# Performance work log

Measured on AMD Instinct MI355X. Metric: run time of the kernel, lower is better.

The kernel has to match this reference:

```python
import jax, jax.numpy as jnp
import numpy as np

B, D_IN, D_H = 4096, 1024, 1024


def setup_inputs() -> dict:
    key = jax.random.key(0)
    ks = jax.random.split(key, 11)
    s = 1.0 / np.sqrt(D_IN + D_H)  # torch Linear default init scale
    inp = {
        "x": jax.random.normal(ks[0], (B, D_IN), jnp.float32),
        "h": jax.random.normal(ks[1], (B, D_H), jnp.float32),
        "c": jax.random.normal(ks[2], (B, D_H), jnp.float32),
        "W_f": jax.random.uniform(ks[3], (D_IN + D_H, D_H), jnp.float32, -s, s),
        "b_f": jax.random.uniform(ks[4], (D_H,), jnp.float32, -s, s),
        "W_i": jax.random.uniform(ks[5], (D_IN + D_H, D_H), jnp.float32, -s, s),
        "b_i": jax.random.uniform(ks[6], (D_H,), jnp.float32, -s, s),
        "W_c": jax.random.uniform(ks[7], (D_IN + D_H, D_H), jnp.float32, -s, s),
        "b_c": jax.random.uniform(ks[8], (D_H,), jnp.float32, -s, s),
        "W_o": jax.random.uniform(ks[9], (D_IN + D_H, D_H), jnp.float32, -s, s),
        "b_o": jax.random.uniform(ks[10], (D_H,), jnp.float32, -s, s),
    }
    return inp


def reference(x, h, c, W_f, b_f, W_i, b_i, W_c, b_c, W_o, b_o):
    xh = jnp.concatenate([x, h], axis=1)  # [B, D_IN+D_H]
    # fuse four gate linears into one GEMM: [B, 2H] @ [2H, 4H]
    W = jnp.concatenate([W_f, W_i, W_c, W_o], axis=1)
    b = jnp.concatenate([b_f, b_i, b_c, b_o], axis=0)
    gates = xh @ W + b  # [B, 4H]
    f_g, i_g, c_g, o_g = jnp.split(gates, 4, axis=1)
    f = jax.nn.sigmoid(f_g)
    i = jax.nn.sigmoid(i_g)
    ct = jnp.tanh(c_g)
    ot = jax.nn.sigmoid(o_g)
    c_new = f * c + i * ct
    h_new = ot * jnp.tanh(c_new)
    return (h_new, (h_new, c_new))
```

## Files before the change

### kernel.cpp

```cpp
#include <hip/hip_runtime.h>
#include <hip/hip_bf16.h>
#include <cstdint>

typedef __bf16 bf16x8 __attribute__((ext_vector_type(8)));
typedef float f32x4 __attribute__((ext_vector_type(4)));

#define BROWS 4096
#define DH    1024
#define KDIM  2048
#define NT    32

__global__ __launch_bounds__(256) void k_prep(const float* __restrict__ x,
                                              const float* __restrict__ h,
                                              const float* __restrict__ Wf,
                                              const float* __restrict__ Wi,
                                              const float* __restrict__ Wc,
                                              const float* __restrict__ Wo,
                                              __hip_bfloat16* __restrict__ xh,
                                              __hip_bfloat16* __restrict__ wt) {
  __shared__ float t[64][65];
  const int tid = threadIdx.x;
  if (blockIdx.x < 4096) {
    int64_t idx = ((int64_t)blockIdx.x * 256 + tid) * 8;
    int row = (int)(idx >> 11);
    int col = (int)(idx & 2047);
    const float* src = (col < 1024) ? (x + (int64_t)row * 1024 + col)
                                    : (h + (int64_t)row * 1024 + (col - 1024));
    float4 v0 = reinterpret_cast<const float4*>(src)[0];
    float4 v1 = reinterpret_cast<const float4*>(src)[1];
    alignas(16) __hip_bfloat16 o8[8];
    o8[0] = __float2bfloat16(v0.x); o8[1] = __float2bfloat16(v0.y);
    o8[2] = __float2bfloat16(v0.z); o8[3] = __float2bfloat16(v0.w);
    o8[4] = __float2bfloat16(v1.x); o8[5] = __float2bfloat16(v1.y);
    o8[6] = __float2bfloat16(v1.z); o8[7] = __float2bfloat16(v1.w);
    *reinterpret_cast<int4*>(xh + idx) = *reinterpret_cast<const int4*>(o8);
  } else {
    const int b = blockIdx.x - 4096;
    const int g  = b & 3;
    const int jt = (b >> 2) & 15;
    const int kt = b >> 6;
    const float* W = (g == 0) ? Wf : (g == 1) ? Wi : (g == 2) ? Wc : Wo;
    const int j0 = jt << 6, k0 = kt << 6;
#pragma unroll
    for (int i = 0; i < 4; ++i) {
      int r = (tid >> 4) + (i << 4);
      int c = (tid & 15) << 2;
      float4 v = *reinterpret_cast<const float4*>(W + (int64_t)(k0 + r) * 1024 + j0 + c);
      t[r][c + 0] = v.x; t[r][c + 1] = v.y; t[r][c + 2] = v.z; t[r][c + 3] = v.w;
    }
    __syncthreads();
#pragma unroll
    for (int i = 0; i < 2; ++i) {
      int task = tid + (i << 8);
      int rr = task >> 3;
      int kc = (task & 7) << 3;
      int np = (((jt << 2) + (rr >> 4)) << 6) + (g << 4) + (rr & 15);
      alignas(16) __hip_bfloat16 o8[8];
#pragma unroll
      for (int e = 0; e < 8; ++e) o8[e] = __float2bfloat16(t[kc + e][rr]);
      *reinterpret_cast<int4*>(wt + (int64_t)np * KDIM + k0 + kc) =
          *reinterpret_cast<const int4*>(o8);
    }
  }
}

__device__ __forceinline__ float sig_(float v) {
  return __builtin_amdgcn_rcpf(1.0f + __expf(-v));
}
__device__ __forceinline__ float tanh_(float v) {
  return fmaf(2.0f, __builtin_amdgcn_rcpf(1.0f + __expf(-2.0f * v)), -1.0f);
}

#define GLD(PTR, LOFF)                                                           \
  __builtin_amdgcn_global_load_lds(                                              \
      (const __attribute__((address_space(1))) void*)(PTR),                      \
      (__attribute__((address_space(3))) void*)(lds + (LOFF) + wslot), 16, 0, 0)

#define STG(P0, P1, LBASE)                                                       \
  do { GLD(P0, (LBASE)); GLD(P1, (LBASE) + 4096); } while (0)

#define LDSA(P, KH, MI)                                                          \
  (*reinterpret_cast<const bf16x8*>(lds + (P) * 32768 + (KH) * 8192 + abase + (MI) * 512))
#define LDSB(P, KH, NI)                                                          \
  (*reinterpret_cast<const bf16x8*>(lds + (P) * 32768 + (KH) * 8192 + bbase + (NI) * 512))

#define VM4 asm volatile("s_waitcnt vmcnt(4)" ::: "memory")
#define NOVM do {} while (0)

#define PHASE(P, KH, MIH, STAGE_STMT, VMSTMT)                                    \
  do {                                                                           \
    bf16x8 av[4];                                                                \
    if ((MIH) == 0) {                                                            \
      _Pragma("unroll") for (int ni = 0; ni < 4; ++ni) bv[ni] = LDSB(P, KH, ni); \
    }                                                                            \
    _Pragma("unroll") for (int i = 0; i < 4; ++i) av[i] = LDSA(P, KH, (MIH) * 4 + i); \
    STAGE_STMT;                                                                  \
    VMSTMT;                                                                      \
    __builtin_amdgcn_s_barrier();                                                \
    __builtin_amdgcn_s_setprio(1);                                               \
    _Pragma("unroll") for (int i = 0; i < 4; ++i)                                \
      _Pragma("unroll") for (int ni = 0; ni < 4; ++ni)                           \
        acc[(MIH) * 4 + i][ni] = __builtin_amdgcn_mfma_f32_16x16x32_bf16(        \
            av[i], bv[ni], acc[(MIH) * 4 + i][ni], 0, 0, 0);                     \
    __builtin_amdgcn_s_setprio(0);                                               \
    __builtin_amdgcn_s_barrier();                                                \
  } while (0)

#define ADV do { a0 += 64; a1 += 64; b0 += 64; b1 += 64; } while (0)

__global__ __launch_bounds__(512, 2) void k_lstm_gemm(
    const __hip_bfloat16* __restrict__ xh, const __hip_bfloat16* __restrict__ wt,
    const float* __restrict__ cin,
    const float* __restrict__ bfp, const float* __restrict__ bip,
    const float* __restrict__ bcp, const float* __restrict__ bop,
    float* __restrict__ out) {
  __shared__ __hip_bfloat16 lds[65536];
  const int tid  = threadIdx.x;
  const int lane = tid & 63;
  const int wid  = tid >> 6;
  const int wm = wid >> 2, wn = wid & 3;
  const int wmb = wm << 7, wnb = wn << 6;

  const int bid  = blockIdx.x;
  const int flat = ((bid & 7) << 5) | (bid >> 3);
  const int m0 = (flat & 15) << 8;
  const int n0 = (flat >> 4) << 8;

  f32x4 acc[8][4] = {};

  const int wslot = wid << 9;
  const int cl = (((lane & 3) ^ ((lane >> 3) & 3)) << 3);
  const __hip_bfloat16* a0 = xh + (int64_t)(m0 + (tid >> 2)) * KDIM + cl;
  const __hip_bfloat16* a1 = a0 + 128 * KDIM;
  const __hip_bfloat16* b0 = wt + (int64_t)(n0 + (tid >> 2)) * KDIM + cl;
  const __hip_bfloat16* b1 = b0 + 128 * KDIM;

  const int frow = lane & 15;
  const int rx   = (((lane >> 4) ^ ((frow >> 1) & 3)) << 3);
  const int abase = ((wmb + frow) << 5) + rx;
  const int bbase = 16384 + ((wnb + frow) << 5) + rx;

  STG(a0, a1, 0);
  STG(b0, b1, 16384);
  STG(a0 + 32, a1 + 32, 8192);
  STG(b0 + 32, b1 + 32, 16384 + 8192);
  ADV;
  asm volatile("s_waitcnt vmcnt(4)" ::: "memory");
  __builtin_amdgcn_s_barrier();

  for (int t = 0; t < NT; t += 2) {
    {
      bf16x8 bv[4];
      PHASE(0, 0, 0, STG(a0, a1, 32768), NOVM);
      PHASE(0, 0, 1, STG(b0, b1, 32768 + 16384), VM4);
      PHASE(0, 1, 0, STG(a0 + 32, a1 + 32, 32768 + 8192), NOVM);
      PHASE(0, 1, 1, STG(b0 + 32, b1 + 32, 32768 + 16384 + 8192), VM4);
    }
    if (t != 30) ADV;
    {
      bf16x8 bv[4];
      PHASE(1, 0, 0, STG(a0, a1, 0), NOVM);
      PHASE(1, 0, 1, STG(b0, b1, 16384), VM4);
      PHASE(1, 1, 0, STG(a0 + 32, a1 + 32, 8192), NOVM);
      PHASE(1, 1, 1, STG(b0 + 32, b1 + 32, 16384 + 8192), VM4);
    }
    ADV;
  }

  const int j = (((n0 >> 6) + wn) << 4) + frow;
  const float vbf = bfp[j], vbi = bip[j], vbc = bcp[j], vbo = bop[j];
  const int q4 = (lane >> 4) << 2;
  float* outh1 = out;
  float* outh2 = out + (int64_t)BROWS * DH;
  float* outc  = out + (int64_t)2 * BROWS * DH;
#pragma unroll
  for (int mi = 0; mi < 8; ++mi) {
    const int mbase = m0 + wmb + (mi << 4) + q4;
#pragma unroll
    for (int r = 0; r < 4; ++r) {
      const int m = mbase + r;
      const int64_t idx = (int64_t)m * DH + j;
      float fg = sig_(acc[mi][0][r] + vbf);
      float ig = sig_(acc[mi][1][r] + vbi);
      float cg = tanh_(acc[mi][2][r] + vbc);
      float og = sig_(acc[mi][3][r] + vbo);
      float cn = fg * cin[idx] + ig * cg;
      float hn = og * tanh_(cn);
      outh1[idx] = hn;
      outh2[idx] = hn;
      outc[idx]  = cn;
    }
  }
}

extern "C" void kernel_launch(void* const* d_in, const int* in_sizes, int n_in,
                              void* d_out, int out_size, void* d_ws, size_t ws_size,
                              hipStream_t stream) {
  const float* x  = (const float*)d_in[0];
  const float* h  = (const float*)d_in[1];
  const float* c  = (const float*)d_in[2];
  const float* Wf = (const float*)d_in[3];
  const float* bf = (const float*)d_in[4];
  const float* Wi = (const float*)d_in[5];
  const float* bi = (const float*)d_in[6];
  const float* Wc = (const float*)d_in[7];
  const float* bc = (const float*)d_in[8];
  const float* Wo = (const float*)d_in[9];
  const float* bo = (const float*)d_in[10];
  float* out = (float*)d_out;

  __hip_bfloat16* xh = (__hip_bfloat16*)d_ws;
  __hip_bfloat16* wt = xh + (int64_t)BROWS * KDIM;

  hipLaunchKernelGGL(k_prep, dim3(6144), dim3(256), 0, stream,
                     x, h, Wf, Wi, Wc, Wo, xh, wt);
  hipLaunchKernelGGL(k_lstm_gemm, dim3(256), dim3(512), 0, stream,
                     xh, wt, c, bf, bi, bc, bo, out);
}
```

Measured before the change: 86.64 us.

## Double-buffer A fragments in registers and cut per-phase barriers in GEMM loop

Restructures the main GEMM loop so the LDS reads for the next phase's A fragments go into a second register bank before the current MFMA block runs. This overlaps LDS reads with matrix math. It also merges the A and B global-to-LDS stage issues into one four-load macro and drops the barrier that sat before each MFMA block, leaving one barrier per block. The cost is extra VGPRs for the second fragment bank, a harder vmcnt/barrier ordering to reason about, and one redundant LDS read after the final iteration.

```diff
diff --git a/kernel.cpp b/kernel.cpp
--- a/kernel.cpp
+++ b/kernel.cpp
@@ -76,8 +76,13 @@
       (const __attribute__((address_space(1))) void*)(PTR),                      \
       (__attribute__((address_space(3))) void*)(lds + (LOFF) + wslot), 16, 0, 0)
 
-#define STG(P0, P1, LBASE)                                                       \
-  do { GLD(P0, (LBASE)); GLD(P1, (LBASE) + 4096); } while (0)
+#define STG2(LP, KH_, PA, PB)                                                    \
+  do {                                                                           \
+    GLD((PA), (LP) + (KH_) * 8192);                                              \
+    GLD((PA) + 128 * KDIM, (LP) + (KH_) * 8192 + 4096);                          \
+    GLD((PB), (LP) + 16384 + (KH_) * 8192);                                      \
+    GLD((PB) + 128 * KDIM, (LP) + 16384 + (KH_) * 8192 + 4096);                  \
+  } while (0)
 
 #define LDSA(P, KH, MI)                                                          \
   (*reinterpret_cast<const bf16x8*>(lds + (P) * 32768 + (KH) * 8192 + abase + (MI) * 512))
@@ -85,28 +90,24 @@
   (*reinterpret_cast<const bf16x8*>(lds + (P) * 32768 + (KH) * 8192 + bbase + (NI) * 512))
 
 #define VM4 asm volatile("s_waitcnt vmcnt(4)" ::: "memory")
-#define NOVM do {} while (0)
-
-#define PHASE(P, KH, MIH, STAGE_STMT, VMSTMT)                                    \
+
+#define RD_AV(BANK, P_, KH_, H_)                                                 \
+  _Pragma("unroll") for (int i = 0; i < 4; ++i) BANK[i] = LDSA(P_, KH_, (H_) * 4 + i)
+#define RD_BV(P_, KH_)                                                           \
+  _Pragma("unroll") for (int ni = 0; ni < 4; ++ni) bv[ni] = LDSB(P_, KH_, ni)
+
+#define MM(BANK, MIH_)                                                           \
   do {                                                                           \
-    bf16x8 av[4];                                                                \
-    if ((MIH) == 0) {                                                            \
-      _Pragma("unroll") for (int ni = 0; ni < 4; ++ni) bv[ni] = LDSB(P, KH, ni); \
-    }                                                                            \
-    _Pragma("unroll") for (int i = 0; i < 4; ++i) av[i] = LDSA(P, KH, (MIH) * 4 + i); \
-    STAGE_STMT;                                                                  \
-    VMSTMT;                                                                      \
-    __builtin_amdgcn_s_barrier();                                                \
     __builtin_amdgcn_s_setprio(1);                                               \
     _Pragma("unroll") for (int i = 0; i < 4; ++i)                                \
       _Pragma("unroll") for (int ni = 0; ni < 4; ++ni)                           \
-        acc[(MIH) * 4 + i][ni] = __builtin_amdgcn_mfma_f32_16x16x32_bf16(        \
-            av[i], bv[ni], acc[(MIH) * 4 + i][ni], 0, 0, 0);                     \
+        acc[(MIH_) * 4 + i][ni] = __builtin_amdgcn_mfma_f32_16x16x32_bf16(       \
+            BANK[i], bv[ni], acc[(MIH_) * 4 + i][ni], 0, 0, 0);                  \
     __builtin_amdgcn_s_setprio(0);                                               \
     __builtin_amdgcn_s_barrier();                                                \
   } while (0)
 
-#define ADV do { a0 += 64; a1 += 64; b0 += 64; b1 += 64; } while (0)
+#define ADV do { a0 += 64; b0 += 64; } while (0)
 
 __global__ __launch_bounds__(512, 2) void k_lstm_gemm(
     const __hip_bfloat16* __restrict__ xh, const __hip_bfloat16* __restrict__ wt,
@@ -131,38 +132,47 @@
   const int wslot = wid << 9;
   const int cl = (((lane & 3) ^ ((lane >> 3) & 3)) << 3);
   const __hip_bfloat16* a0 = xh + (int64_t)(m0 + (tid >> 2)) * KDIM + cl;
-  const __hip_bfloat16* a1 = a0 + 128 * KDIM;
   const __hip_bfloat16* b0 = wt + (int64_t)(n0 + (tid >> 2)) * KDIM + cl;
-  const __hip_bfloat16* b1 = b0 + 128 * KDIM;
 
   const int frow = lane & 15;
   const int rx   = (((lane >> 4) ^ ((frow >> 1) & 3)) << 3);
   const int abase = ((wmb + frow) << 5) + rx;
   const int bbase = 16384 + ((wnb + frow) << 5) + rx;
 
-  STG(a0, a1, 0);
-  STG(b0, b1, 16384);
-  STG(a0 + 32, a1 + 32, 8192);
-  STG(b0 + 32, b1 + 32, 16384 + 8192);
+  bf16x8 avA[4], avB[4], bv[4];
+
+  STG2(0, 0, a0, b0);
+  STG2(0, 1, a0 + 32, b0 + 32);
   ADV;
-  asm volatile("s_waitcnt vmcnt(4)" ::: "memory");
+  VM4;
   __builtin_amdgcn_s_barrier();
+  RD_AV(avA, 0, 0, 0);
 
   for (int t = 0; t < NT; t += 2) {
     {
-      bf16x8 bv[4];
-      PHASE(0, 0, 0, STG(a0, a1, 32768), NOVM);
-      PHASE(0, 0, 1, STG(b0, b1, 32768 + 16384), VM4);
-      PHASE(0, 1, 0, STG(a0 + 32, a1 + 32, 32768 + 8192), NOVM);
-      PHASE(0, 1, 1, STG(b0 + 32, b1 + 32, 32768 + 16384 + 8192), VM4);
+      RD_BV(0, 0); RD_AV(avB, 0, 0, 1);
+      STG2(32768, 0, a0, b0);
+      VM4; MM(avA, 0);
+      RD_AV(avA, 0, 1, 0);
+      STG2(32768, 1, a0 + 32, b0 + 32);
+      MM(avB, 1);
+      RD_BV(0, 1); RD_AV(avB, 0, 1, 1);
+      VM4; MM(avA, 0);
+      RD_AV(avA, 1, 0, 0);
+      MM(avB, 1);
     }
     if (t != 30) ADV;
     {
-      bf16x8 bv[4];
-      PHASE(1, 0, 0, STG(a0, a1, 0), NOVM);
-      PHASE(1, 0, 1, STG(b0, b1, 16384), VM4);
-      PHASE(1, 1, 0, STG(a0 + 32, a1 + 32, 8192), NOVM);
-      PHASE(1, 1, 1, STG(b0 + 32, b1 + 32, 16384 + 8192), VM4);
+      RD_BV(1, 0); RD_AV(avB, 1, 0, 1);
+      STG2(0, 0, a0, b0);
+      VM4; MM(avA, 0);
+      RD_AV(avA, 1, 1, 0);
+      STG2(0, 1, a0 + 32, b0 + 32);
+      MM(avB, 1);
+      RD_BV(1, 1); RD_AV(avB, 1, 1, 1);
+      VM4; MM(avA, 0);
+      RD_AV(avA, 0, 0, 0);
+      MM(avB, 1);
     }
     ADV;
   }
```

Result: no change. 87.66 us (+1.2%).
